# Optimization experiments

Measured on AMD Instinct MI355X. Metric: run time of the kernel, lower is better.

Reference implementation:

```python
import jax, jax.numpy as jnp
import numpy as np

N = 100000      # nodes
E = 1600000     # edges
G = 1024        # graphs in batch
H = 128         # graph_hidden
F_IN = 38
DEPTH = 4
EPS = 1e-5


def setup_inputs() -> dict:
    key = jax.random.key(0)
    ks = jax.random.split(key, 16)
    inp = {
        "h": jax.random.normal(ks[0], (N, F_IN), jnp.float32),
        "src": jax.random.randint(ks[1], (E,), 0, N, jnp.int32),
        "dst": jax.random.randint(ks[2], (E,), 0, N, jnp.int32),
        "node2graph": jnp.sort(jax.random.randint(ks[3], (N,), 0, G, jnp.int32)),
        "W1": jax.random.normal(ks[4], (F_IN, H), jnp.float32) * 0.1,
        "b1": jnp.zeros((H,), jnp.float32),
        "g1": jnp.ones((H,), jnp.float32),
        "be1": jnp.zeros((H,), jnp.float32),
        "W2s": jax.random.normal(ks[5], (DEPTH - 1, H, H), jnp.float32) * 0.1,
        "b2s": jnp.zeros((DEPTH - 1, H), jnp.float32),
        "g2s": jnp.ones((DEPTH - 1, H), jnp.float32),
        "be2s": jnp.zeros((DEPTH - 1, H), jnp.float32),
        "aw": jax.random.normal(ks[6], (H, 1), jnp.float32) * 0.1,
        "ab": jnp.zeros((1,), jnp.float32),
        "Wf1": jax.random.normal(ks[7], (H, 512), jnp.float32) * 0.1,
        "bf1": jnp.zeros((512,), jnp.float32),
        "gf1": jnp.ones((512,), jnp.float32),
        "bef1": jnp.zeros((512,), jnp.float32),
        "Wl": jax.random.normal(ks[8], (512, 256), jnp.float32) * 0.05,
        "bl": jnp.zeros((256,), jnp.float32),
        "gl": jnp.ones((256,), jnp.float32),
        "bel": jnp.zeros((256,), jnp.float32),
        "Wf2": jax.random.normal(ks[9], (256, 67), jnp.float32) * 0.05,
        "bf2": jnp.zeros((67,), jnp.float32),
    }
    return inp


def _bn(x, g, b):
    # BatchNorm1d in training mode: batch stats (biased variance), eps=1e-5.
    m = jnp.mean(x, axis=0)
    v = jnp.mean(jnp.square(x - m), axis=0)
    return g * (x - m) * jax.lax.rsqrt(v + EPS) + b


def reference(h, src, dst, node2graph,
              W1, b1, g1, be1, W2s, b2s, g2s, be2s,
              aw, ab, Wf1, bf1, gf1, bef1, Wl, bl, gl, bel, Wf2, bf2):
    ones_e = jnp.ones((E,), h.dtype)
    deg_out = jax.ops.segment_sum(ones_e, src, num_segments=N)
    deg_in = jax.ops.segment_sum(ones_e, dst, num_segments=N)
    ns = jax.lax.rsqrt(jnp.maximum(deg_out, 1.0))  # src-side D^{-1/2}
    nd = jax.lax.rsqrt(jnp.maximum(deg_in, 1.0))   # dst-side D^{-1/2}

    def gconv(x, W, b):
        # DGL GraphConv norm='both': D_dst^{-1/2} A D_src^{-1/2} x W + b
        msg = (x * ns[:, None])[src]                      # [E, F] gather
        agg = jax.ops.segment_sum(msg, dst, num_segments=N)
        return (agg * nd[:, None]) @ W + b

    # dropout p = 0.0 -> identity
    x = jax.nn.relu(_bn(gconv(h, W1, b1), g1, be1))
    for i in range(DEPTH - 1):
        x = jax.nn.relu(_bn(gconv(x, W2s[i], b2s[i]), g2s[i], be2s[i]))

    # WeightAndSum readout: sigmoid-gated segment sum over nodes per graph
    atom_weights = x @ aw + ab                            # [N, 1] (pre-sigmoid, returned)
    w = jax.nn.sigmoid(atom_weights)
    hg = jax.ops.segment_sum(x * w, node2graph, num_segments=G)  # [G, H]

    y = jax.nn.relu(_bn(hg @ Wf1 + bf1, gf1, bef1))
    y = jax.nn.relu(_bn(y @ Wl + bl, gl, bel))
    y = jax.nn.sigmoid(y @ Wf2 + bf2)                     # [G, 67]
    return (y, atom_weights)
```

## Files before the change

kernel.cpp:

```cpp
#include <hip/hip_runtime.h>
#include <math.h>

#define NN 100000
#define NE 1600000
#define NG 1024
#define MAXDEG 64
#define EPSB 1e-5f

#define NBUK 1563
#define NBLK 256
#define EPB  6250
#define FLAT (2*NBUK*NBLK)
#define NCH  ((FLAT + 1023)/1024)

typedef _Float16 h16;
typedef __attribute__((ext_vector_type(2))) _Float16 h16x2;
typedef __attribute__((ext_vector_type(4))) _Float16 h16x4;
typedef __attribute__((ext_vector_type(8))) _Float16 h16x8;
typedef __attribute__((ext_vector_type(4))) float f32x4;

static __device__ __forceinline__ float sigmoidf_(float x){ return 1.f/(1.f+__expf(-x)); }

__global__ __launch_bounds__(512)
void k_hist(const int* __restrict__ src, const int* __restrict__ dst,
            int* __restrict__ blockHist){
  __shared__ int hd[NBUK];
  __shared__ int hs[NBUK];
  int b = blockIdx.x, t = threadIdx.x;
  for (int j = t; j < NBUK; j += 512){ hd[j] = 0; hs[j] = 0; }
  __syncthreads();
  int e0 = b*EPB, e1 = e0 + EPB;
  for (int i = e0 + t; i < e1; i += 512){
    atomicAdd(&hd[dst[i]>>6], 1);
    atomicAdd(&hs[src[i]>>6], 1);
  }
  __syncthreads();
  for (int j = t; j < NBUK; j += 512){
    blockHist[(size_t)j*NBLK + b] = hd[j];
    blockHist[(size_t)(NBUK + j)*NBLK + b] = hs[j];
  }
}

__global__ __launch_bounds__(256)
void k_scan1(int* __restrict__ data, int* __restrict__ csum){
  __shared__ int s[256];
  int blk = blockIdx.x, t = threadIdx.x;
  int base = blk*1024 + t*4;
  int v0=0,v1=0,v2=0,v3=0;
  if (base+0 < FLAT) v0 = data[base+0];
  if (base+1 < FLAT) v1 = data[base+1];
  if (base+2 < FLAT) v2 = data[base+2];
  if (base+3 < FLAT) v3 = data[base+3];
  int tot = v0+v1+v2+v3;
  s[t] = tot; __syncthreads();
  for (int o=1;o<256;o<<=1){ int x = (t>=o)? s[t-o]:0; __syncthreads(); s[t]+=x; __syncthreads(); }
  int excl = s[t] - tot;
  if (t == 255) csum[blk] = s[255];
  if (base+0 < FLAT) data[base+0] = excl;
  if (base+1 < FLAT) data[base+1] = excl + v0;
  if (base+2 < FLAT) data[base+2] = excl + v0 + v1;
  if (base+3 < FLAT) data[base+3] = excl + v0 + v1 + v2;
}

__global__ void k_scan2(int* __restrict__ csum){
  __shared__ int s[1024];
  int t = threadIdx.x;
  int x = (t < NCH) ? csum[t] : 0;
  s[t] = x; __syncthreads();
  for (int o=1;o<1024;o<<=1){ int y = (t>=o)? s[t-o]:0; __syncthreads(); s[t]+=y; __syncthreads(); }
  if (t < NCH) csum[t] = s[t] - x;
}

static __device__ __forceinline__ int rd_scanned(const int* data, const int* csum, int idx){
  return data[idx] + csum[idx >> 10];
}

__global__ __launch_bounds__(512)
void k_scatter(const int* __restrict__ src, const int* __restrict__ dst,
               const int* __restrict__ scanned, const int* __restrict__ csum,
               unsigned int* __restrict__ sortedBuf){
  __shared__ int bd[NBUK];
  __shared__ int bs[NBUK];
  int b = blockIdx.x, t = threadIdx.x;
  for (int j = t; j < NBUK; j += 512){
    bd[j] = rd_scanned(scanned, csum, j*NBLK + b);
    bs[j] = rd_scanned(scanned, csum, (NBUK + j)*NBLK + b);
  }
  __syncthreads();
  int e0 = b*EPB, e1 = e0 + EPB;
  for (int i = e0 + t; i < e1; i += 512){
    int s = src[i], d = dst[i];
    int posD = atomicAdd(&bd[d>>6], 1);
    sortedBuf[posD] = (unsigned int)s | ((unsigned int)(d & 63) << 20);
    int posS = atomicAdd(&bs[s>>6], 1);
    sortedBuf[posS] = (unsigned int)s;
  }
}

__global__ __launch_bounds__(256)
void k_build(const unsigned int* __restrict__ sortedBuf, const int* __restrict__ scanned,
             const int* __restrict__ csum, const float* __restrict__ h,
             int* __restrict__ eidx, int* __restrict__ degI,
             float* __restrict__ ns, float* __restrict__ nd, h16* __restrict__ hn){
  __shared__ int cnt[64];
  __shared__ float nsl[64];
  int k = blockIdx.x, t = threadIdx.x;
  int v0 = k*64;
  int nv = NN - v0; if (nv > 64) nv = 64;
  if (t < 64) cnt[t] = 0;
  __syncthreads();
  int startD = rd_scanned(scanned, csum, k*NBLK);
  int endD   = rd_scanned(scanned, csum, (k+1)*NBLK);
  for (int i = startD + t; i < endD; i += 256){
    unsigned int u = sortedBuf[i];
    int lid = (int)(u >> 20);
    int slot = atomicAdd(&cnt[lid], 1);
    if (slot < MAXDEG) eidx[(size_t)(v0 + lid)*MAXDEG + slot] = (int)(u & 0xFFFFFu);
  }
  __syncthreads();
  if (t < nv){
    int v = v0 + t;
    int dI = cnt[t];
    degI[v] = dI;
    nd[v] = rsqrtf(fmaxf((float)dI, 1.f));
    int c = dI > MAXDEG ? MAXDEG : dI;
    int ad = (c + 7) & ~7; if (ad < 8) ad = 8; if (ad > MAXDEG) ad = MAXDEG;
    for (int i = c; i < ad; i++) eidx[(size_t)v*MAXDEG + i] = NN;
  }
  __syncthreads();
  if (t < 64) cnt[t] = 0;
  __syncthreads();
  int startS = rd_scanned(scanned, csum, (NBUK + k)*NBLK);
  int endS   = (k+1 < NBUK) ? rd_scanned(scanned, csum, (NBUK + k + 1)*NBLK) : 2*NE;
  for (int i = startS + t; i < endS; i += 256){
    atomicAdd(&cnt[sortedBuf[i] & 63u], 1);
  }
  __syncthreads();
  if (t < 64){
    float nsv = 0.f;
    if (t < nv){
      nsv = rsqrtf(fmaxf((float)cnt[t], 1.f));
      ns[v0 + t] = nsv;
    }
    nsl[t] = nsv;
  }
  __syncthreads();
  for (int i = t; i < 64*64; i += 256){
    int r = i >> 6, c = i & 63;
    int v = v0 + r;
    if (v < NN){
      float val = (c < 38) ? h[(size_t)v*38 + c]*nsl[r] : 0.f;
      hn[(size_t)v*64 + c] = (h16)val;
    }
  }
  if (k == 0){
    for (int i = t; i < 64; i += 256) hn[(size_t)NN*64 + i] = (h16)0.f;
  }
}

__global__ void k_prepg(const int* __restrict__ n2g,
                        int* __restrict__ gs, int* __restrict__ ge, float* __restrict__ stats,
                        float* __restrict__ ns, h16* __restrict__ XA, h16* __restrict__ XB){
  int v = blockIdx.x*256 + threadIdx.x;
  if (v < NN){
    int g = n2g[v];
    if (v == 0){
      for (int q = 0; q <= g; q++) gs[q] = 0;
      for (int q = 0; q < g; q++) ge[q] = 0;
    } else {
      int gp = n2g[v-1];
      if (gp != g){
        for (int q = gp+1; q <= g; q++) gs[q] = v;
        for (int q = gp; q < g; q++) ge[q] = v;
      }
    }
    if (v == NN-1){
      for (int q = g+1; q < NG; q++) gs[q] = NN;
      for (int q = g; q < NG; q++) ge[q] = NN;
    }
  }
  if (v == NN) ns[NN] = 0.f;
  if (blockIdx.x == 0){
    int t = threadIdx.x;
    for (int j = t; j < 4096; j += 256) stats[j] = 0.f;
    if (t < 128){ XA[(size_t)NN*128 + t] = (h16)0.f; XB[(size_t)NN*128 + t] = (h16)0.f; }
  }
}

__global__ void k_convall(const float* __restrict__ W1, const float* __restrict__ W2s,
                          const float* __restrict__ Wf1, const float* __restrict__ Wl,
                          h16* __restrict__ W1t, h16* __restrict__ W2t,
                          h16* __restrict__ Wf1t, h16* __restrict__ Wlt){
  int i = blockIdx.x*256 + threadIdx.x;
  if (i < 8192){
    int c = i >> 6, k = i & 63;
    W1t[i] = (k < 38) ? (h16)W1[(size_t)k*128 + c] : (h16)0.f;
  } else if (i < 57344){
    int j = i - 8192; int l = j >> 14; int r = j & 16383;
    int c = r >> 7, k = r & 127;
    W2t[j] = (h16)W2s[(size_t)l*16384 + (size_t)k*128 + c];
  } else if (i < 122880){
    int j = i - 57344; int c = j >> 7, k = j & 127;
    Wf1t[j] = (h16)Wf1[(size_t)k*512 + c];
  } else if (i < 253952){
    int j = i - 122880; int c = j >> 9, k = j & 511;
    Wlt[j] = (h16)Wl[(size_t)k*256 + c];
  }
}

__global__ __launch_bounds__(256)
void k_gs40(const h16* __restrict__ hn, const int* __restrict__ eidx,
            const int* __restrict__ degI, const float* __restrict__ nd,
            h16* __restrict__ A38){
  int v = (blockIdx.x*256 + threadIdx.x) >> 6;
  int lane = threadIdx.x & 63;
  if (v >= NN) return;
  int deg = degI[v]; if (deg > MAXDEG) deg = MAXDEG;
  int deg8 = (deg + 7) & ~7; if (deg8 < 8) deg8 = 8; if (deg8 > MAXDEG) deg8 = MAXDEG;
  const int* row = eidx + (size_t)v*MAXDEG;
  int g = lane / 20;
  int c0 = 2*(lane % 20);
  bool act = (lane < 40);
  int gg = g & 1;
  float a0 = 0.f, a1 = 0.f;
  int4 s4 = *(const int4*)(row + 4*gg);
  h16x2 u0={}, u1={}, u2={}, u3={};
  if (act){
    u0 = *(const h16x2*)(hn + (size_t)s4.x*64 + c0);
    u1 = *(const h16x2*)(hn + (size_t)s4.y*64 + c0);
    u2 = *(const h16x2*)(hn + (size_t)s4.z*64 + c0);
    u3 = *(const h16x2*)(hn + (size_t)s4.w*64 + c0);
  }
  for (int e = 0; e < deg8; e += 8){
    int nx = (e + 8 < deg8) ? e + 8 : e;
    int4 s4n = *(const int4*)(row + nx + 4*gg);
    h16x2 n0={}, n1={}, n2={}, n3={};
    if (act){
      n0 = *(const h16x2*)(hn + (size_t)s4n.x*64 + c0);
      n1 = *(const h16x2*)(hn + (size_t)s4n.y*64 + c0);
      n2 = *(const h16x2*)(hn + (size_t)s4n.z*64 + c0);
      n3 = *(const h16x2*)(hn + (size_t)s4n.w*64 + c0);
    }
    a0 += ((float)u0[0] + (float)u1[0]) + ((float)u2[0] + (float)u3[0]);
    a1 += ((float)u0[1] + (float)u1[1]) + ((float)u2[1] + (float)u3[1]);
    u0=n0; u1=n1; u2=n2; u3=n3;
  }
  float b0 = __shfl(a0, lane + 20);
  float b1 = __shfl(a1, lane + 20);
  if (lane < 20){
    float ndv = nd[v];
    h16x2 o; o[0] = (h16)((a0 + b0)*ndv); o[1] = (h16)((a1 + b1)*ndv);
    *(h16x2*)(A38 + (size_t)v*64 + c0) = o;
  } else if (lane < 32){
    h16x2 o; o[0] = (h16)0.f; o[1] = (h16)0.f;
    *(h16x2*)(A38 + (size_t)v*64 + 40 + 2*(lane - 20)) = o;
  }
}

__global__ __launch_bounds__(256)
void k_gs128(const h16* __restrict__ X, const int* __restrict__ eidx,
             const int* __restrict__ degI, const float* __restrict__ ns,
             const float* __restrict__ nd, const float* __restrict__ stats,
             const float* __restrict__ gam, const float* __restrict__ bet,
             h16* __restrict__ agg){
  __shared__ float scs[128], shs[128];
  int t = threadIdx.x;
  if (t < 128){
    float m = stats[t]*(1.f/(float)NN);
    float var = fmaxf(stats[128+t]*(1.f/(float)NN) - m*m, 0.f);
    float inv = rsqrtf(var + EPSB);
    float sc = gam[t]*inv;
    scs[t] = sc; shs[t] = fmaf(-sc, m, bet[t]);
  }
  __syncthreads();
  int v = (blockIdx.x*256 + t) >> 6;
  int lane = t & 63;
  if (v >= NN) return;
  int deg = degI[v]; if (deg > MAXDEG) deg = MAXDEG;
  int deg8 = (deg + 7) & ~7; if (deg8 < 8) deg8 = 8; if (deg8 > MAXDEG) deg8 = MAXDEG;
  const int* row = eidx + (size_t)v*MAXDEG;
  int half = lane >> 5;
  int c0 = 4*(lane & 31);
  float4 sc = *(const float4*)&scs[c0];
  float4 sh = *(const float4*)&shs[c0];
  float a0=0.f, a1=0.f, a2=0.f, a3=0.f;
  int4 s4 = *(const int4*)(row + 4*half);
  float w0=ns[s4.x], w1=ns[s4.y], w2=ns[s4.z], w3=ns[s4.w];
  h16x4 u0 = *(const h16x4*)(X + (size_t)s4.x*128 + c0);
  h16x4 u1 = *(const h16x4*)(X + (size_t)s4.y*128 + c0);
  h16x4 u2 = *(const h16x4*)(X + (size_t)s4.z*128 + c0);
  h16x4 u3 = *(const h16x4*)(X + (size_t)s4.w*128 + c0);
  for (int e = 0; e < deg8; e += 8){
    int nx = (e + 8 < deg8) ? e + 8 : e;
    int4 s4n = *(const int4*)(row + nx + 4*half);
    float v0=ns[s4n.x], v1=ns[s4n.y], v2=ns[s4n.z], v3=ns[s4n.w];
    h16x4 n0 = *(const h16x4*)(X + (size_t)s4n.x*128 + c0);
    h16x4 n1 = *(const h16x4*)(X + (size_t)s4n.y*128 + c0);
    h16x4 n2 = *(const h16x4*)(X + (size_t)s4n.z*128 + c0);
    h16x4 n3 = *(const h16x4*)(X + (size_t)s4n.w*128 + c0);
    a0 = fmaf(fmaxf(fmaf((float)u0[0], sc.x, sh.x), 0.f), w0, a0);
    a1 = fmaf(fmaxf(fmaf((float)u0[1], sc.y, sh.y), 0.f), w0, a1);
    a2 = fmaf(fmaxf(fmaf((float)u0[2], sc.z, sh.z), 0.f), w0, a2);
    a3 = fmaf(fmaxf(fmaf((float)u0[3], sc.w, sh.w), 0.f), w0, a3);
    a0 = fmaf(fmaxf(fmaf((float)u1[0], sc.x, sh.x), 0.f), w1, a0);
    a1 = fmaf(fmaxf(fmaf((float)u1[1], sc.y, sh.y), 0.f), w1, a1);
    a2 = fmaf(fmaxf(fmaf((float)u1[2], sc.z, sh.z), 0.f), w1, a2);
    a3 = fmaf(fmaxf(fmaf((float)u1[3], sc.w, sh.w), 0.f), w1, a3);
    a0 = fmaf(fmaxf(fmaf((float)u2[0], sc.x, sh.x), 0.f), w2, a0);
    a1 = fmaf(fmaxf(fmaf((float)u2[1], sc.y, sh.y), 0.f), w2, a1);
    a2 = fmaf(fmaxf(fmaf((float)u2[2], sc.z, sh.z), 0.f), w2, a2);
    a3 = fmaf(fmaxf(fmaf((float)u2[3], sc.w, sh.w), 0.f), w2, a3);
    a0 = fmaf(fmaxf(fmaf((float)u3[0], sc.x, sh.x), 0.f), w3, a0);
    a1 = fmaf(fmaxf(fmaf((float)u3[1], sc.y, sh.y), 0.f), w3, a1);
    a2 = fmaf(fmaxf(fmaf((float)u3[2], sc.z, sh.z), 0.f), w3, a2);
    a3 = fmaf(fmaxf(fmaf((float)u3[3], sc.w, sh.w), 0.f), w3, a3);
    u0=n0; u1=n1; u2=n2; u3=n3;
    w0=v0; w1=v1; w2=v2; w3=v3;
  }
  a0 += __shfl_xor(a0, 32);
  a1 += __shfl_xor(a1, 32);
  a2 += __shfl_xor(a2, 32);
  a3 += __shfl_xor(a3, 32);
  if (half == 0){
    float ndv = nd[v];
    h16x4 o;
    o[0] = (h16)(a0*ndv); o[1] = (h16)(a1*ndv);
    o[2] = (h16)(a2*ndv); o[3] = (h16)(a3*ndv);
    *(h16x4*)(agg + (size_t)v*128 + c0) = o;
  }
}

__global__ __launch_bounds__(256)
void k_mgemm(const h16* __restrict__ A, const h16* __restrict__ Wt,
             const float* __restrict__ bias, h16* __restrict__ Cout,
             float* __restrict__ stats, int M, int K, int Nc){
  __shared__ h16 As[128][72];
  __shared__ h16 Bs[128][72];
  __shared__ float sred[2][128];
  int m0 = blockIdx.x*128, n0 = blockIdx.y*128;
  int t = threadIdx.x, w = t>>6, lane = t&63;
  int wr = (w>>1)*64, wc = (w&1)*64;
  f32x4 acc[4][4] = {};

  int ar = t>>3;
  int ac = (t&7)*8;
  for (int k0=0; k0<K; k0+=64){
    #pragma unroll
    for (int rr=0; rr<128; rr+=32){
      int gm = m0 + ar + rr;
      h16x8 val = {};
      if (gm < M) val = *(const h16x8*)(A + (size_t)gm*K + k0 + ac);
      *(h16x8*)&As[ar+rr][ac] = val;
    }
    #pragma unroll
    for (int rr=0; rr<128; rr+=32){
      int gc = n0 + ar + rr;
      h16x8 val = {};
      if (gc < Nc) val = *(const h16x8*)(Wt + (size_t)gc*K + k0 + ac);
      *(h16x8*)&Bs[ar+rr][ac] = val;
    }
    __syncthreads();
    int rsel = lane & 15;
    #pragma unroll
    for (int kk=0; kk<64; kk+=32){
      int ksel = kk + (lane>>4)*8;
      h16x8 af[4], bfr[4];
      #pragma unroll
      for (int i=0;i<4;i++) af[i]  = *(const h16x8*)&As[wr + i*16 + rsel][ksel];
      #pragma unroll
      for (int j=0;j<4;j++) bfr[j] = *(const h16x8*)&Bs[wc + j*16 + rsel][ksel];
      #pragma unroll
      for (int i=0;i<4;i++)
        #pragma unroll
        for (int j=0;j<4;j++)
          acc[i][j] = __builtin_amdgcn_mfma_f32_16x16x32_f16(af[i], bfr[j], acc[i][j], 0, 0, 0);
    }
    __syncthreads();
  }

  float csum[4] = {}, csq[4] = {};
  int colsel = lane & 15, rowsel = (lane>>4)*4;
  #pragma unroll
  for (int j=0;j<4;j++){
    int gc = n0 + wc + j*16 + colsel;
    float bv = (gc < Nc) ? bias[gc] : 0.f;
    #pragma unroll
    for (int i=0;i<4;i++){
      #pragma unroll
      for (int r=0;r<4;r++){
        int gm = m0 + wr + i*16 + rowsel + r;
        if (gm < M && gc < Nc){
          float v = acc[i][j][r] + bv;
          Cout[(size_t)gm*Nc + gc] = (h16)v;
          csum[j] += v; csq[j] += v*v;
        }
      }
    }
  }
  if (stats){
    ((float*)sred)[t] = 0.f;
    __syncthreads();
    #pragma unroll
    for (int j=0;j<4;j++){
      int lc = wc + j*16 + colsel;
      atomicAdd(&sred[0][lc], csum[j]);
      atomicAdd(&sred[1][lc], csq[j]);
    }
    __syncthreads();
    if (t < 128){
      int gc = n0 + t;
      if (gc < Nc){
        atomicAdd(&stats[gc],      sred[0][t]);
        atomicAdd(&stats[Nc + gc], sred[1][t]);
      }
    }
  }
}

__global__ __launch_bounds__(256)
void k_mgemmbn(const h16* __restrict__ A, const h16* __restrict__ Wt,
               const float* __restrict__ bias, h16* __restrict__ Cout,
               float* __restrict__ statsOut, const float* __restrict__ statsIn,
               const float* __restrict__ gam, const float* __restrict__ bet,
               float invM, int M, int K, int Nc){
  __shared__ float scs[512], shs[512];
  __shared__ h16 As[128][72];
  __shared__ h16 Bs[128][72];
  __shared__ float sred[2][128];
  int t = threadIdx.x;
  for (int c = t; c < K; c += 256){
    float m = statsIn[c]*invM;
    float var = fmaxf(statsIn[K+c]*invM - m*m, 0.f);
    float inv = rsqrtf(var + EPSB);
    float sc = gam[c]*inv;
    scs[c] = sc; shs[c] = fmaf(-sc, m, bet[c]);
  }
  __syncthreads();
  int m0 = blockIdx.x*128, n0 = blockIdx.y*128;
  int w = t>>6, lane = t&63;
  int wr = (w>>1)*64, wc = (w&1)*64;
  f32x4 acc[4][4] = {};

  int ar = t>>3;
  int ac = (t&7)*8;
  for (int k0=0; k0<K; k0+=64){
    #pragma unroll
    for (int rr=0; rr<128; rr+=32){
      int gm = m0 + ar + rr;
      h16x8 val = {};
      if (gm < M){
        h16x8 raw = *(const h16x8*)(A + (size_t)gm*K + k0 + ac);
        #pragma unroll
        for (int j=0;j<8;j++){
          int kk = k0 + ac + j;
          val[j] = (h16)fmaxf(fmaf((float)raw[j], scs[kk], shs[kk]), 0.f);
        }
      }
      *(h16x8*)&As[ar+rr][ac] = val;
    }
    #pragma unroll
    for (int rr=0; rr<128; rr+=32){
      int gc = n0 + ar + rr;
      h16x8 val = {};
      if (gc < Nc) val = *(const h16x8*)(Wt + (size_t)gc*K + k0 + ac);
      *(h16x8*)&Bs[ar+rr][ac] = val;
    }
    __syncthreads();
    int rsel = lane & 15;
    #pragma unroll
    for (int kk=0; kk<64; kk+=32){
      int ksel = kk + (lane>>4)*8;
      h16x8 af[4], bfr[4];
      #pragma unroll
      for (int i=0;i<4;i++) af[i]  = *(const h16x8*)&As[wr + i*16 + rsel][ksel];
      #pragma unroll
      for (int j=0;j<4;j++) bfr[j] = *(const h16x8*)&Bs[wc + j*16 + rsel][ksel];
      #pragma unroll
      for (int i=0;i<4;i++)
        #pragma unroll
        for (int j=0;j<4;j++)
          acc[i][j] = __builtin_amdgcn_mfma_f32_16x16x32_f16(af[i], bfr[j], acc[i][j], 0, 0, 0);
    }
    __syncthreads();
  }

  float csum[4] = {}, csq[4] = {};
  int colsel = lane & 15, rowsel = (lane>>4)*4;
  #pragma unroll
  for (int j=0;j<4;j++){
    int gc = n0 + wc + j*16 + colsel;
    float bv = (gc < Nc) ? bias[gc] : 0.f;
    #pragma unroll
    for (int i=0;i<4;i++){
      #pragma unroll
      for (int r=0;r<4;r++){
        int gm = m0 + wr + i*16 + rowsel + r;
        if (gm < M && gc < Nc){
          float v = acc[i][j][r] + bv;
          Cout[(size_t)gm*Nc + gc] = (h16)v;
          csum[j] += v; csq[j] += v*v;
        }
      }
    }
  }
  ((float*)sred)[t] = 0.f;
  __syncthreads();
  #pragma unroll
  for (int j=0;j<4;j++){
    int lc = wc + j*16 + colsel;
    atomicAdd(&sred[0][lc], csum[j]);
    atomicAdd(&sred[1][lc], csq[j]);
  }
  __syncthreads();
  if (t < 128){
    int gc = n0 + t;
    if (gc < Nc){
      atomicAdd(&statsOut[gc],      sred[0][t]);
      atomicAdd(&statsOut[Nc + gc], sred[1][t]);
    }
  }
}

__global__ __launch_bounds__(256)
void k_readout(const h16* __restrict__ X, const float* __restrict__ stats,
               const float* __restrict__ gam, const float* __restrict__ bet,
               const float* __restrict__ aw, const float* __restrict__ ab,
               const int* __restrict__ gs, const int* __restrict__ ge,
               float* __restrict__ awout, h16* __restrict__ hg){
  __shared__ float scs[128], shs[128], awv[128];
  __shared__ float red[4][128];
  int t = threadIdx.x;
  if (t < 128){
    float m = stats[t]*(1.f/(float)NN);
    float var = fmaxf(stats[128+t]*(1.f/(float)NN) - m*m, 0.f);
    float inv = rsqrtf(var + EPSB);
    float sc = gam[t]*inv;
    scs[t] = sc; shs[t] = fmaf(-sc, m, bet[t]);
    awv[t] = aw[t];
  }
  __syncthreads();
  int g = blockIdx.x;
  int s = gs[g], e = ge[g];
  int w = t>>6, lane = t&63, c0 = 2*lane;
  float sc0=scs[c0], sc1=scs[c0+1], sh0=shs[c0], sh1=shs[c0+1];
  float aw0=awv[c0], aw1=awv[c0+1];
  float ab0 = ab[0];
  float acc0=0.f, acc1=0.f;
  for (int n = s + w; n < e; n += 4){
    h16x2 u = *(const h16x2*)(X + (size_t)n*128 + c0);
    float x0 = fmaxf(fmaf((float)u[0], sc0, sh0), 0.f);
    float x1 = fmaxf(fmaf((float)u[1], sc1, sh1), 0.f);
    float d = x0*aw0 + x1*aw1;
    #pragma unroll
    for (int o=32;o>0;o>>=1) d += __shfl_xor(d, o);
    float tv = d + ab0;
    if (lane == 0) awout[n] = tv;
    float wn = sigmoidf_(tv);
    acc0 = fmaf(x0, wn, acc0);
    acc1 = fmaf(x1, wn, acc1);
  }
  red[w][c0] = acc0; red[w][c0+1] = acc1;
  __syncthreads();
  if (w == 0){
    float a0 = red[0][c0] + red[1][c0] + red[2][c0] + red[3][c0];
    float a1 = red[0][c0+1] + red[1][c0+1] + red[2][c0+1] + red[3][c0+1];
    h16x2 o; o[0] = (h16)a0; o[1] = (h16)a1;
    *(h16x2*)(hg + (size_t)g*128 + c0) = o;
  }
}

__global__ __launch_bounds__(256)
void k_finalbn(const h16* __restrict__ y2p, const float* __restrict__ Wf2,
               const float* __restrict__ bf2v, const float* __restrict__ statsIn,
               const float* __restrict__ gam, const float* __restrict__ bet,
               float* __restrict__ out){
  __shared__ float scs[256], shs[256];
  int t = threadIdx.x;
  {
    float m = statsIn[t]*(1.f/(float)NG);
    float var = fmaxf(statsIn[256+t]*(1.f/(float)NG) - m*m, 0.f);
    float inv = rsqrtf(var + EPSB);
    float sc = gam[t]*inv;
    scs[t] = sc; shs[t] = fmaf(-sc, m, bet[t]);
  }
  __syncthreads();
  int idx = blockIdx.x*256 + t;
  if (idx >= NG*67) return;
  int g = idx / 67, c = idx % 67;
  float s = bf2v[c];
  const h16* row = y2p + (size_t)g*256;
  for (int k=0;k<256;k+=2){
    h16x2 u = *(const h16x2*)(row + k);
    float x0 = fmaxf(fmaf((float)u[0], scs[k],   shs[k]),   0.f);
    float x1 = fmaxf(fmaf((float)u[1], scs[k+1], shs[k+1]), 0.f);
    s = fmaf(x0, Wf2[(size_t)k*67 + c], s);
    s = fmaf(x1, Wf2[(size_t)(k+1)*67 + c], s);
  }
  out[(size_t)g*67 + c] = sigmoidf_(s);
}

extern "C" void kernel_launch(void* const* d_in, const int* in_sizes, int n_in,
                              void* d_out, int out_size, void* d_ws, size_t ws_size,
                              hipStream_t stream){
  const float* h   = (const float*)d_in[0];
  const int*   src = (const int*)d_in[1];
  const int*   dst = (const int*)d_in[2];
  const int*   n2g = (const int*)d_in[3];
  const float* W1  = (const float*)d_in[4];
  const float* b1  = (const float*)d_in[5];
  const float* g1  = (const float*)d_in[6];
  const float* be1 = (const float*)d_in[7];
  const float* W2s = (const float*)d_in[8];
  const float* b2s = (const float*)d_in[9];
  const float* g2s = (const float*)d_in[10];
  const float* be2s= (const float*)d_in[11];
  const float* aw  = (const float*)d_in[12];
  const float* ab  = (const float*)d_in[13];
  const float* Wf1 = (const float*)d_in[14];
  const float* bf1 = (const float*)d_in[15];
  const float* gf1 = (const float*)d_in[16];
  const float* bef1= (const float*)d_in[17];
  const float* Wl  = (const float*)d_in[18];
  const float* bl  = (const float*)d_in[19];
  const float* gl  = (const float*)d_in[20];
  const float* bel = (const float*)d_in[21];
  const float* Wf2 = (const float*)d_in[22];
  const float* bf2v= (const float*)d_in[23];
  float* out = (float*)d_out;

  char* p = (char*)d_ws;
  auto carve = [&](size_t bytes)->void*{
    void* r = (void*)p; p += (bytes + 255) & ~(size_t)255; return r;
  };
  h16* XA   = (h16*)carve((size_t)(NN+1)*128*2);
  h16* XB   = (h16*)carve((size_t)(NN+1)*128*2);
  h16* hn   = (h16*)carve((size_t)(NN+1)*64*2);
  h16* A38  = (h16*)carve((size_t)NN*64*2);
  int* eidx = (int*)carve((size_t)NN*MAXDEG*4);
  unsigned int* sortedBuf = (unsigned int*)carve((size_t)2*NE*4);
  int* blockHist = (int*)carve((size_t)FLAT*4);
  int* csum = (int*)carve(1024*4);
  int* degI = (int*)carve((size_t)NN*4);
  float* ns = (float*)carve((size_t)(NN+1)*4);
  float* nd = (float*)carve((size_t)NN*4);
  int* gsge = (int*)carve((size_t)2*NG*4);
  h16* hg   = (h16*)carve((size_t)NG*128*2);
  h16* y1p  = (h16*)carve((size_t)NG*512*2);
  h16* y2p  = (h16*)carve((size_t)NG*256*2);
  float* stats = (float*)carve(4096*4);
  h16* W1t  = (h16*)carve((size_t)128*64*2);
  h16* W2t  = (h16*)carve((size_t)3*128*128*2);
  h16* Wf1t = (h16*)carve((size_t)512*128*2);
  h16* Wlt  = (h16*)carve((size_t)256*512*2);

  int* gs = gsge;
  int* ge = gsge + NG;
  float* st1  = stats;
  float* st2a = stats + 256;
  float* st2b = stats + 512;
  float* st2c = stats + 768;
  float* stf1 = stats + 1024;
  float* stl  = stats + 2048;
  float* st2[3] = { st2a, st2b, st2c };

  k_convall<<<(253952+255)/256, 256, 0, stream>>>(W1, W2s, Wf1, Wl, W1t, W2t, Wf1t, Wlt);
  k_prepg  <<<(NN+1+255)/256, 256, 0, stream>>>(n2g, gs, ge, stats, ns, XA, XB);

  k_hist   <<<NBLK, 512, 0, stream>>>(src, dst, blockHist);
  k_scan1  <<<NCH, 256, 0, stream>>>(blockHist, csum);
  k_scan2  <<<1, 1024, 0, stream>>>(csum);
  k_scatter<<<NBLK, 512, 0, stream>>>(src, dst, blockHist, csum, sortedBuf);
  k_build  <<<NBUK, 256, 0, stream>>>(sortedBuf, blockHist, csum, h, eidx, degI, ns, nd, hn);

  const int nodeBlocks = (NN + 3)/4;
  const int gemmBlocks = (NN + 127)/128;

  k_gs40 <<<nodeBlocks, 256, 0, stream>>>(hn, eidx, degI, nd, A38);
  k_mgemm<<<dim3(gemmBlocks,1), 256, 0, stream>>>(A38, W1t, b1, XA, st1, NN, 64, 128);

  const float* stPrev[3] = { st1, st2a, st2b };
  const float* gPrev[3]  = { g1, g2s, g2s + 128 };
  const float* bePrev[3] = { be1, be2s, be2s + 128 };
  for (int i=0;i<3;i++){
    k_gs128<<<nodeBlocks, 256, 0, stream>>>(XA, eidx, degI, ns, nd,
                                            stPrev[i], gPrev[i], bePrev[i], XB);
    k_mgemm<<<dim3(gemmBlocks,1), 256, 0, stream>>>(XB, W2t + (size_t)i*128*128, b2s + i*128,
                                                    XA, st2[i], NN, 128, 128);
  }

  k_readout<<<NG, 256, 0, stream>>>(XA, st2c, g2s + 256, be2s + 256, aw, ab,
                                    gs, ge, out + (size_t)NG*67, hg);

  k_mgemm  <<<dim3(NG/128, 4), 256, 0, stream>>>(hg, Wf1t, bf1, y1p, stf1, NG, 128, 512);
  k_mgemmbn<<<dim3(NG/128, 2), 256, 0, stream>>>(y1p, Wlt, bl, y2p, stl, stf1, gf1, bef1,
                                                 1.0f/(float)NG, NG, 512, 256);
  k_finalbn<<<(NG*67+255)/256, 256, 0, stream>>>(y2p, Wf2, bf2v, stl, gl, bel, out);
}
```

Before: 650.4 us.

## Use CSR adjacency and feature-sliced layout for cache-friendly gathers

Replaces the padded fixed-width (64 slots per node) edge table with a compact CSR array built from per-block prefix sums, and stores node features in 8 column slices of 16 halves each so every gather block touches only a 3.2MB slice of X. The aggregation kernel is split per slice, and a new GEMM writes its output directly in the sliced layout. The goal is better L2 hit rates and no padding reads during the random neighbour gathers. In exchange, the readout kernel has to read the strided slice layout, and each gather now moves only 8-byte pieces per neighbour with more blocks.

```diff
diff --git a/kernel.cpp b/kernel.cpp
--- a/kernel.cpp
+++ b/kernel.cpp
@@ -4,8 +4,8 @@
 #define NN 100000
 #define NE 1600000
 #define NG 1024
-#define MAXDEG 64
 #define EPSB 1e-5f
+#define NNP (NN+1)
 
 #define NBUK 1563
 #define NBLK 256
@@ -100,46 +100,60 @@
 __global__ __launch_bounds__(256)
 void k_build(const unsigned int* __restrict__ sortedBuf, const int* __restrict__ scanned,
              const int* __restrict__ csum, const float* __restrict__ h,
-             int* __restrict__ eidx, int* __restrict__ degI,
+             int* __restrict__ eidxC, int* __restrict__ off, int* __restrict__ degI,
              float* __restrict__ ns, float* __restrict__ nd, h16* __restrict__ hn){
   __shared__ int cnt[64];
+  __shared__ int excl[64];
+  __shared__ int cnt2[64];
   __shared__ float nsl[64];
   int k = blockIdx.x, t = threadIdx.x;
   int v0 = k*64;
   int nv = NN - v0; if (nv > 64) nv = 64;
-  if (t < 64) cnt[t] = 0;
+  if (t < 64){ cnt[t] = 0; cnt2[t] = 0; }
   __syncthreads();
   int startD = rd_scanned(scanned, csum, k*NBLK);
   int endD   = rd_scanned(scanned, csum, (k+1)*NBLK);
   for (int i = startD + t; i < endD; i += 256){
-    unsigned int u = sortedBuf[i];
-    int lid = (int)(u >> 20);
-    int slot = atomicAdd(&cnt[lid], 1);
-    if (slot < MAXDEG) eidx[(size_t)(v0 + lid)*MAXDEG + slot] = (int)(u & 0xFFFFFu);
-  }
-  __syncthreads();
+    atomicAdd(&cnt[sortedBuf[i] >> 20], 1);
+  }
+  __syncthreads();
+  if (t < 64) excl[t] = cnt[t];
+  __syncthreads();
+  #pragma unroll
+  for (int o = 1; o < 64; o <<= 1){
+    int x = 0;
+    if (t < 64 && t >= o) x = excl[t-o];
+    __syncthreads();
+    if (t < 64) excl[t] += x;
+    __syncthreads();
+  }
   if (t < nv){
     int v = v0 + t;
     int dI = cnt[t];
     degI[v] = dI;
+    off[v] = startD + excl[t] - dI;
     nd[v] = rsqrtf(fmaxf((float)dI, 1.f));
-    int c = dI > MAXDEG ? MAXDEG : dI;
-    int ad = (c + 7) & ~7; if (ad < 8) ad = 8; if (ad > MAXDEG) ad = MAXDEG;
-    for (int i = c; i < ad; i++) eidx[(size_t)v*MAXDEG + i] = NN;
-  }
-  __syncthreads();
-  if (t < 64) cnt[t] = 0;
+  }
+  __syncthreads();
+  for (int i = startD + t; i < endD; i += 256){
+    unsigned int u = sortedBuf[i];
+    int lid = (int)(u >> 20);
+    int slot = atomicAdd(&cnt2[lid], 1);
+    eidxC[startD + (excl[lid] - cnt[lid]) + slot] = (int)(u & 0xFFFFFu);
+  }
+  __syncthreads();
+  if (t < 64) cnt2[t] = 0;
   __syncthreads();
   int startS = rd_scanned(scanned, csum, (NBUK + k)*NBLK);
   int endS   = (k+1 < NBUK) ? rd_scanned(scanned, csum, (NBUK + k + 1)*NBLK) : 2*NE;
   for (int i = startS + t; i < endS; i += 256){
-    atomicAdd(&cnt[sortedBuf[i] & 63u], 1);
+    atomicAdd(&cnt2[sortedBuf[i] & 63u], 1);
   }
   __syncthreads();
   if (t < 64){
     float nsv = 0.f;
     if (t < nv){
-      nsv = rsqrtf(fmaxf((float)cnt[t], 1.f));
+      nsv = rsqrtf(fmaxf((float)cnt2[t], 1.f));
       ns[v0 + t] = nsv;
     }
     nsl[t] = nsv;
@@ -183,7 +197,11 @@
   if (blockIdx.x == 0){
     int t = threadIdx.x;
     for (int j = t; j < 4096; j += 256) stats[j] = 0.f;
-    if (t < 128){ XA[(size_t)NN*128 + t] = (h16)0.f; XB[(size_t)NN*128 + t] = (h16)0.f; }
+    if (t < 128){
+      int s = t >> 4, c = t & 15;
+      XA[((size_t)s*NNP + NN)*16 + c] = (h16)0.f;
+      XB[((size_t)s*NNP + NN)*16 + c] = (h16)0.f;
+    }
   }
 }
 
@@ -209,124 +227,174 @@
 }
 
 __global__ __launch_bounds__(256)
-void k_gs40(const h16* __restrict__ hn, const int* __restrict__ eidx,
-            const int* __restrict__ degI, const float* __restrict__ nd,
-            h16* __restrict__ A38){
+void k_gs40(const h16* __restrict__ hn, const int* __restrict__ eidxC,
+            const int* __restrict__ off, const int* __restrict__ degI,
+            const float* __restrict__ nd, h16* __restrict__ A38){
   int v = (blockIdx.x*256 + threadIdx.x) >> 6;
   int lane = threadIdx.x & 63;
   if (v >= NN) return;
-  int deg = degI[v]; if (deg > MAXDEG) deg = MAXDEG;
-  int deg8 = (deg + 7) & ~7; if (deg8 < 8) deg8 = 8; if (deg8 > MAXDEG) deg8 = MAXDEG;
-  const int* row = eidx + (size_t)v*MAXDEG;
-  int g = lane / 20;
-  int c0 = 2*(lane % 20);
-  bool act = (lane < 40);
-  int gg = g & 1;
-  float a0 = 0.f, a1 = 0.f;
-  int4 s4 = *(const int4*)(row + 4*gg);
-  h16x2 u0={}, u1={}, u2={}, u3={};
-  if (act){
-    u0 = *(const h16x2*)(hn + (size_t)s4.x*64 + c0);
-    u1 = *(const h16x2*)(hn + (size_t)s4.y*64 + c0);
-    u2 = *(const h16x2*)(hn + (size_t)s4.z*64 + c0);
-    u3 = *(const h16x2*)(hn + (size_t)s4.w*64 + c0);
-  }
-  for (int e = 0; e < deg8; e += 8){
-    int nx = (e + 8 < deg8) ? e + 8 : e;
-    int4 s4n = *(const int4*)(row + nx + 4*gg);
-    h16x2 n0={}, n1={}, n2={}, n3={};
-    if (act){
-      n0 = *(const h16x2*)(hn + (size_t)s4n.x*64 + c0);
-      n1 = *(const h16x2*)(hn + (size_t)s4n.y*64 + c0);
-      n2 = *(const h16x2*)(hn + (size_t)s4n.z*64 + c0);
-      n3 = *(const h16x2*)(hn + (size_t)s4n.w*64 + c0);
-    }
-    a0 += ((float)u0[0] + (float)u1[0]) + ((float)u2[0] + (float)u3[0]);
-    a1 += ((float)u0[1] + (float)u1[1]) + ((float)u2[1] + (float)u3[1]);
-    u0=n0; u1=n1; u2=n2; u3=n3;
-  }
-  float b0 = __shfl(a0, lane + 20);
-  float b1 = __shfl(a1, lane + 20);
-  if (lane < 20){
-    float ndv = nd[v];
-    h16x2 o; o[0] = (h16)((a0 + b0)*ndv); o[1] = (h16)((a1 + b1)*ndv);
-    *(h16x2*)(A38 + (size_t)v*64 + c0) = o;
-  } else if (lane < 32){
-    h16x2 o; o[0] = (h16)0.f; o[1] = (h16)0.f;
-    *(h16x2*)(A38 + (size_t)v*64 + 40 + 2*(lane - 20)) = o;
-  }
-}
-
-__global__ __launch_bounds__(256)
-void k_gs128(const h16* __restrict__ X, const int* __restrict__ eidx,
-             const int* __restrict__ degI, const float* __restrict__ ns,
-             const float* __restrict__ nd, const float* __restrict__ stats,
-             const float* __restrict__ gam, const float* __restrict__ bet,
-             h16* __restrict__ agg){
-  __shared__ float scs[128], shs[128];
-  int t = threadIdx.x;
-  if (t < 128){
-    float m = stats[t]*(1.f/(float)NN);
-    float var = fmaxf(stats[128+t]*(1.f/(float)NN) - m*m, 0.f);
-    float inv = rsqrtf(var + EPSB);
-    float sc = gam[t]*inv;
-    scs[t] = sc; shs[t] = fmaf(-sc, m, bet[t]);
-  }
-  __syncthreads();
-  int v = (blockIdx.x*256 + t) >> 6;
-  int lane = t & 63;
-  if (v >= NN) return;
-  int deg = degI[v]; if (deg > MAXDEG) deg = MAXDEG;
-  int deg8 = (deg + 7) & ~7; if (deg8 < 8) deg8 = 8; if (deg8 > MAXDEG) deg8 = MAXDEG;
-  const int* row = eidx + (size_t)v*MAXDEG;
-  int half = lane >> 5;
-  int c0 = 4*(lane & 31);
-  float4 sc = *(const float4*)&scs[c0];
-  float4 sh = *(const float4*)&shs[c0];
+  int cc = lane & 15, g = lane >> 4;
+  int deg = degI[v], base = off[v];
   float a0=0.f, a1=0.f, a2=0.f, a3=0.f;
-  int4 s4 = *(const int4*)(row + 4*half);
-  float w0=ns[s4.x], w1=ns[s4.y], w2=ns[s4.z], w3=ns[s4.w];
-  h16x4 u0 = *(const h16x4*)(X + (size_t)s4.x*128 + c0);
-  h16x4 u1 = *(const h16x4*)(X + (size_t)s4.y*128 + c0);
-  h16x4 u2 = *(const h16x4*)(X + (size_t)s4.z*128 + c0);
-  h16x4 u3 = *(const h16x4*)(X + (size_t)s4.w*128 + c0);
-  for (int e = 0; e < deg8; e += 8){
-    int nx = (e + 8 < deg8) ? e + 8 : e;
-    int4 s4n = *(const int4*)(row + nx + 4*half);
-    float v0=ns[s4n.x], v1=ns[s4n.y], v2=ns[s4n.z], v3=ns[s4n.w];
-    h16x4 n0 = *(const h16x4*)(X + (size_t)s4n.x*128 + c0);
-    h16x4 n1 = *(const h16x4*)(X + (size_t)s4n.y*128 + c0);
-    h16x4 n2 = *(const h16x4*)(X + (size_t)s4n.z*128 + c0);
-    h16x4 n3 = *(const h16x4*)(X + (size_t)s4n.w*128 + c0);
-    a0 = fmaf(fmaxf(fmaf((float)u0[0], sc.x, sh.x), 0.f), w0, a0);
-    a1 = fmaf(fmaxf(fmaf((float)u0[1], sc.y, sh.y), 0.f), w0, a1);
-    a2 = fmaf(fmaxf(fmaf((float)u0[2], sc.z, sh.z), 0.f), w0, a2);
-    a3 = fmaf(fmaxf(fmaf((float)u0[3], sc.w, sh.w), 0.f), w0, a3);
-    a0 = fmaf(fmaxf(fmaf((float)u1[0], sc.x, sh.x), 0.f), w1, a0);
-    a1 = fmaf(fmaxf(fmaf((float)u1[1], sc.y, sh.y), 0.f), w1, a1);
-    a2 = fmaf(fmaxf(fmaf((float)u1[2], sc.z, sh.z), 0.f), w1, a2);
-    a3 = fmaf(fmaxf(fmaf((float)u1[3], sc.w, sh.w), 0.f), w1, a3);
-    a0 = fmaf(fmaxf(fmaf((float)u2[0], sc.x, sh.x), 0.f), w2, a0);
-    a1 = fmaf(fmaxf(fmaf((float)u2[1], sc.y, sh.y), 0.f), w2, a1);
-    a2 = fmaf(fmaxf(fmaf((float)u2[2], sc.z, sh.z), 0.f), w2, a2);
-    a3 = fmaf(fmaxf(fmaf((float)u2[3], sc.w, sh.w), 0.f), w2, a3);
-    a0 = fmaf(fmaxf(fmaf((float)u3[0], sc.x, sh.x), 0.f), w3, a0);
-    a1 = fmaf(fmaxf(fmaf((float)u3[1], sc.y, sh.y), 0.f), w3, a1);
-    a2 = fmaf(fmaxf(fmaf((float)u3[2], sc.z, sh.z), 0.f), w3, a2);
-    a3 = fmaf(fmaxf(fmaf((float)u3[3], sc.w, sh.w), 0.f), w3, a3);
-    u0=n0; u1=n1; u2=n2; u3=n3;
-    w0=v0; w1=v1; w2=v2; w3=v3;
-  }
-  a0 += __shfl_xor(a0, 32);
-  a1 += __shfl_xor(a1, 32);
-  a2 += __shfl_xor(a2, 32);
-  a3 += __shfl_xor(a3, 32);
-  if (half == 0){
+  int e = g;
+  int sv = (e < deg) ? eidxC[base + e] : NN;
+  for (; e < deg; e += 4){
+    int e2 = e + 4;
+    int sv2 = (e2 < deg) ? eidxC[base + e2] : NN;
+    h16x4 u = *(const h16x4*)(hn + (size_t)sv*64 + cc*4);
+    a0 += (float)u[0]; a1 += (float)u[1]; a2 += (float)u[2]; a3 += (float)u[3];
+    sv = sv2;
+  }
+  a0 += __shfl_xor(a0,16); a1 += __shfl_xor(a1,16);
+  a2 += __shfl_xor(a2,16); a3 += __shfl_xor(a3,16);
+  a0 += __shfl_xor(a0,32); a1 += __shfl_xor(a1,32);
+  a2 += __shfl_xor(a2,32); a3 += __shfl_xor(a3,32);
+  if (g == 0){
     float ndv = nd[v];
     h16x4 o;
-    o[0] = (h16)(a0*ndv); o[1] = (h16)(a1*ndv);
-    o[2] = (h16)(a2*ndv); o[3] = (h16)(a3*ndv);
-    *(h16x4*)(agg + (size_t)v*128 + c0) = o;
+    o[0]=(h16)(a0*ndv); o[1]=(h16)(a1*ndv);
+    o[2]=(h16)(a2*ndv); o[3]=(h16)(a3*ndv);
+    *(h16x4*)(A38 + (size_t)v*64 + cc*4) = o;
+  }
+}
+
+__global__ __launch_bounds__(256)
+void k_gs128s(const h16* __restrict__ Xs, const int* __restrict__ eidxC,
+              const int* __restrict__ off, const int* __restrict__ degI,
+              const float* __restrict__ ns, const float* __restrict__ nd,
+              const float* __restrict__ stats, const float* __restrict__ gam,
+              const float* __restrict__ bet, h16* __restrict__ agg){
+  __shared__ float scs[16], shs[16];
+  int slice = blockIdx.x & 7;
+  int chunk = blockIdx.x >> 3;
+  int t = threadIdx.x;
+  if (t < 16){
+    int c = slice*16 + t;
+    float m = stats[c]*(1.f/(float)NN);
+    float var = fmaxf(stats[128+c]*(1.f/(float)NN) - m*m, 0.f);
+    float inv = rsqrtf(var + EPSB);
+    float sc = gam[c]*inv;
+    scs[t] = sc; shs[t] = fmaf(-sc, m, bet[c]);
+  }
+  __syncthreads();
+  int w = t>>6, lane = t&63;
+  int cc = lane & 3;
+  int g  = (lane>>2) & 3;
+  int nsub = lane>>4;
+  float4 sc4 = *(const float4*)&scs[cc*4];
+  float4 sh4 = *(const float4*)&shs[cc*4];
+  const h16* Xb = Xs + (size_t)slice*NNP*16;
+  for (int vv = w*4; vv < 64; vv += 16){
+    int v = chunk*64 + vv + nsub;
+    bool vok = v < NN;
+    int deg = vok ? degI[v] : 0;
+    int base = vok ? off[v] : 0;
+    float a0=0.f, a1=0.f, a2=0.f, a3=0.f;
+    int e = g;
+    int sv = (e < deg) ? eidxC[base + e] : NN;
+    for (; e < deg; e += 4){
+      int e2 = e + 4;
+      int sv2 = (e2 < deg) ? eidxC[base + e2] : NN;
+      float wv = ns[sv];
+      h16x4 u = *(const h16x4*)(Xb + (size_t)sv*16 + cc*4);
+      a0 = fmaf(fmaxf(fmaf((float)u[0], sc4.x, sh4.x), 0.f), wv, a0);
+      a1 = fmaf(fmaxf(fmaf((float)u[1], sc4.y, sh4.y), 0.f), wv, a1);
+      a2 = fmaf(fmaxf(fmaf((float)u[2], sc4.z, sh4.z), 0.f), wv, a2);
+      a3 = fmaf(fmaxf(fmaf((float)u[3], sc4.w, sh4.w), 0.f), wv, a3);
+      sv = sv2;
+    }
+    a0 += __shfl_xor(a0, 4); a1 += __shfl_xor(a1, 4);
+    a2 += __shfl_xor(a2, 4); a3 += __shfl_xor(a3, 4);
+    a0 += __shfl_xor(a0, 8); a1 += __shfl_xor(a1, 8);
+    a2 += __shfl_xor(a2, 8); a3 += __shfl_xor(a3, 8);
+    if (g == 0 && vok){
+      float ndv = nd[v];
+      h16x4 o;
+      o[0]=(h16)(a0*ndv); o[1]=(h16)(a1*ndv);
+      o[2]=(h16)(a2*ndv); o[3]=(h16)(a3*ndv);
+      *(h16x4*)(agg + (size_t)v*128 + slice*16 + cc*4) = o;
+    }
+  }
+}
+
+__global__ __launch_bounds__(256)
+void k_mgemmS(const h16* __restrict__ A, const h16* __restrict__ Wt,
+              const float* __restrict__ bias, h16* __restrict__ Cout,
+              float* __restrict__ stats, int M, int K){
+  __shared__ h16 As[128][72];
+  __shared__ h16 Bs[128][72];
+  __shared__ float sred[2][128];
+  int m0 = blockIdx.x*128;
+  int t = threadIdx.x, w = t>>6, lane = t&63;
+  int wr = (w>>1)*64, wc = (w&1)*64;
+  f32x4 acc[4][4] = {};
+
+  int ar = t>>3;
+  int ac = (t&7)*8;
+  for (int k0=0; k0<K; k0+=64){
+    #pragma unroll
+    for (int rr=0; rr<128; rr+=32){
+      int gm = m0 + ar + rr;
+      h16x8 val = {};
+      if (gm < M) val = *(const h16x8*)(A + (size_t)gm*K + k0 + ac);
+      *(h16x8*)&As[ar+rr][ac] = val;
+    }
+    #pragma unroll
+    for (int rr=0; rr<128; rr+=32){
+      int gc = ar + rr;
+      *(h16x8*)&Bs[gc][ac] = *(const h16x8*)(Wt + (size_t)gc*K + k0 + ac);
+    }
+    __syncthreads();
+    int rsel = lane & 15;
+    #pragma unroll
+    for (int kk=0; kk<64; kk+=32){
+      int ksel = kk + (lane>>4)*8;
+      h16x8 af[4], bfr[4];
+      #pragma unroll
+      for (int i=0;i<4;i++) af[i]  = *(const h16x8*)&As[wr + i*16 + rsel][ksel];
+      #pragma unroll
+      for (int j=0;j<4;j++) bfr[j] = *(const h16x8*)&Bs[wc + j*16 + rsel][ksel];
+      #pragma unroll
+      for (int i=0;i<4;i++)
+        #pragma unroll
+        for (int j=0;j<4;j++)
+          acc[i][j] = __builtin_amdgcn_mfma_f32_16x16x32_f16(af[i], bfr[j], acc[i][j], 0, 0, 0);
+    }
+    __syncthreads();
+  }
+
+  float csum[4] = {}, csq[4] = {};
+  int colsel = lane & 15, rowsel = (lane>>4)*4;
+  #pragma unroll
+  for (int j=0;j<4;j++){
+    int gc = wc + j*16 + colsel;
+    float bv = bias[gc];
+    int s = gc >> 4, c = gc & 15;
+    #pragma unroll
+    for (int i=0;i<4;i++){
+      #pragma unroll
+      for (int r=0;r<4;r++){
+        int gm = m0 + wr + i*16 + rowsel + r;
+        if (gm < M){
+          float v = acc[i][j][r] + bv;
+          Cout[((size_t)s*NNP + gm)*16 + c] = (h16)v;
+          csum[j] += v; csq[j] += v*v;
+        }
+      }
+    }
+  }
+  ((float*)sred)[t] = 0.f;
+  __syncthreads();
+  #pragma unroll
+  for (int j=0;j<4;j++){
+    int lc = wc + j*16 + colsel;
+    atomicAdd(&sred[0][lc], csum[j]);
+    atomicAdd(&sred[1][lc], csq[j]);
+  }
+  __syncthreads();
+  if (t < 128){
+    atomicAdd(&stats[t],       sred[0][t]);
+    atomicAdd(&stats[128 + t], sred[1][t]);
   }
 }
 
@@ -545,9 +613,10 @@
   float sc0=scs[c0], sc1=scs[c0+1], sh0=shs[c0], sh1=shs[c0+1];
   float aw0=awv[c0], aw1=awv[c0+1];
   float ab0 = ab[0];
+  size_t sliceBase = ((size_t)(c0>>4)*NNP)*16 + (c0&15);
   float acc0=0.f, acc1=0.f;
   for (int n = s + w; n < e; n += 4){
-    h16x2 u = *(const h16x2*)(X + (size_t)n*128 + c0);
+    h16x2 u = *(const h16x2*)(X + sliceBase + (size_t)n*16);
     float x0 = fmaxf(fmaf((float)u[0], sc0, sh0), 0.f);
     float x1 = fmaxf(fmaf((float)u[1], sc1, sh1), 0.f);
     float d = x0*aw0 + x1*aw1;
@@ -632,16 +701,17 @@
   auto carve = [&](size_t bytes)->void*{
     void* r = (void*)p; p += (bytes + 255) & ~(size_t)255; return r;
   };
-  h16* XA   = (h16*)carve((size_t)(NN+1)*128*2);
-  h16* XB   = (h16*)carve((size_t)(NN+1)*128*2);
-  h16* hn   = (h16*)carve((size_t)(NN+1)*64*2);
+  h16* XA   = (h16*)carve((size_t)NNP*128*2);
+  h16* XB   = (h16*)carve((size_t)NNP*128*2);
+  h16* hn   = (h16*)carve((size_t)NNP*64*2);
   h16* A38  = (h16*)carve((size_t)NN*64*2);
-  int* eidx = (int*)carve((size_t)NN*MAXDEG*4);
+  int* eidxC = (int*)carve((size_t)NE*4);
+  int* off   = (int*)carve((size_t)NN*4);
   unsigned int* sortedBuf = (unsigned int*)carve((size_t)2*NE*4);
   int* blockHist = (int*)carve((size_t)FLAT*4);
   int* csum = (int*)carve(1024*4);
   int* degI = (int*)carve((size_t)NN*4);
-  float* ns = (float*)carve((size_t)(NN+1)*4);
+  float* ns = (float*)carve((size_t)NNP*4);
   float* nd = (float*)carve((size_t)NN*4);
   int* gsge = (int*)carve((size_t)2*NG*4);
   h16* hg   = (h16*)carve((size_t)NG*128*2);
@@ -670,22 +740,24 @@
   k_scan1  <<<NCH, 256, 0, stream>>>(blockHist, csum);
   k_scan2  <<<1, 1024, 0, stream>>>(csum);
   k_scatter<<<NBLK, 512, 0, stream>>>(src, dst, blockHist, csum, sortedBuf);
-  k_build  <<<NBUK, 256, 0, stream>>>(sortedBuf, blockHist, csum, h, eidx, degI, ns, nd, hn);
+  k_build  <<<NBUK, 256, 0, stream>>>(sortedBuf, blockHist, csum, h,
+                                      eidxC, off, degI, ns, nd, hn);
 
   const int nodeBlocks = (NN + 3)/4;
   const int gemmBlocks = (NN + 127)/128;
-
-  k_gs40 <<<nodeBlocks, 256, 0, stream>>>(hn, eidx, degI, nd, A38);
-  k_mgemm<<<dim3(gemmBlocks,1), 256, 0, stream>>>(A38, W1t, b1, XA, st1, NN, 64, 128);
+  const int sliceBlocks = 8*NBUK;
+
+  k_gs40 <<<nodeBlocks, 256, 0, stream>>>(hn, eidxC, off, degI, nd, A38);
+  k_mgemmS<<<gemmBlocks, 256, 0, stream>>>(A38, W1t, b1, XA, st1, NN, 64);
 
   const float* stPrev[3] = { st1, st2a, st2b };
   const float* gPrev[3]  = { g1, g2s, g2s + 128 };
   const float* bePrev[3] = { be1, be2s, be2s + 128 };
   for (int i=0;i<3;i++){
-    k_gs128<<<nodeBlocks, 256, 0, stream>>>(XA, eidx, degI, ns, nd,
-                                            stPrev[i], gPrev[i], bePrev[i], XB);
-    k_mgemm<<<dim3(gemmBlocks,1), 256, 0, stream>>>(XB, W2t + (size_t)i*128*128, b2s + i*128,
-                                                    XA, st2[i], NN, 128, 128);
+    k_gs128s<<<sliceBlocks, 256, 0, stream>>>(XA, eidxC, off, degI, ns, nd,
+                                              stPrev[i], gPrev[i], bePrev[i], XB);
+    k_mgemmS<<<gemmBlocks, 256, 0, stream>>>(XB, W2t + (size_t)i*128*128, b2s + i*128,
+                                             XA, st2[i], NN, 128);
   }
 
   k_readout<<<NG, 256, 0, stream>>>(XA, st2c, g2s + 256, be2s + 256, aw, ab,
```

New measurement: 894.7 us. 37.6% more time.
